# Kernel optimization log

Measured on AMD Instinct MI355X. Metric: run time of the kernel, lower is better.

## Reference

```python
import jax, jax.numpy as jnp
import numpy as np

NEG_SLOPE = 0.2  # PyG GATConv default leaky_relu slope

def gat_conv(x, src, dst, W, att_src, att_dst, bias, concat):
    # x: [N, F_in]; W: [F_in, H*D]; att_*: [H, D]; edges src->dst
    N = x.shape[0]
    H, D = att_src.shape
    h = (x @ W).reshape(N, H, D)                      # [N, H, D]
    a_src = (h * att_src[None]).sum(-1)               # [N, H]
    a_dst = (h * att_dst[None]).sum(-1)               # [N, H]
    e = jax.nn.leaky_relu(a_src[src] + a_dst[dst], NEG_SLOPE)  # [E, H]
    # segment softmax over incoming edges of each destination node
    emax = jax.ops.segment_max(e, dst, num_segments=N)          # [N, H]
    emax = jnp.where(jnp.isfinite(emax), emax, 0.0)
    ex = jnp.exp(e - emax[dst])                                  # [E, H]
    denom = jax.ops.segment_sum(ex, dst, num_segments=N)        # [N, H]
    alpha = ex / (denom[dst] + 1e-16)                            # [E, H]
    msg = h[src] * alpha[:, :, None]                             # [E, H, D]
    out = jax.ops.segment_sum(msg, dst, num_segments=N)          # [N, H, D]
    out = out.reshape(N, H * D) if concat else out.mean(axis=1)
    return out + bias

def setup_inputs() -> dict:
    key = jax.random.key(0)
    ks = jax.random.split(key, 10)
    N, F_in, E, H, D, C = 100000, 128, 3200000, 8, 8, 7
    x = jax.random.normal(ks[0], (N, F_in), jnp.float32)
    edge_index = jax.random.randint(ks[1], (2, E), 0, N, jnp.int64)
    W1 = jax.random.normal(ks[2], (F_in, H * D), jnp.float32) / np.sqrt(F_in)
    att_src1 = jax.random.normal(ks[3], (H, D), jnp.float32) / np.sqrt(D)
    att_dst1 = jax.random.normal(ks[4], (H, D), jnp.float32) / np.sqrt(D)
    b1 = jax.random.normal(ks[5], (H * D,), jnp.float32) * 0.01
    W2 = jax.random.normal(ks[6], (H * D, C), jnp.float32) / np.sqrt(H * D)
    att_src2 = jax.random.normal(ks[7], (1, C), jnp.float32) / np.sqrt(C)
    att_dst2 = jax.random.normal(ks[8], (1, C), jnp.float32) / np.sqrt(C)
    b2 = jax.random.normal(ks[9], (C,), jnp.float32) * 0.01
    return {"x": x, "edge_index": edge_index, "W1": W1, "att_src1": att_src1,
            "att_dst1": att_dst1, "b1": b1, "W2": W2, "att_src2": att_src2,
            "att_dst2": att_dst2, "b2": b2}

def reference(x, edge_index, W1, att_src1, att_dst1, b1, W2, att_src2, att_dst2, b2):
    N = x.shape[0]
    # PyG GATConv add_self_loops=True
    loop = jnp.arange(N, dtype=edge_index.dtype)
    src = jnp.concatenate([edge_index[0], loop])
    dst = jnp.concatenate([edge_index[1], loop])
    # eval mode: dropouts are no-ops
    h = gat_conv(x, src, dst, W1, att_src1, att_dst1, b1, concat=True)
    emb = h
    h = jax.nn.elu(h)
    logits = gat_conv(h, src, dst, W2, att_src2, att_dst2, b2, concat=False)
    return emb, jax.nn.log_softmax(logits, axis=1)
```

## Files before the change

### kernel.cpp

```cpp
#include <hip/hip_runtime.h>
#include <hip/hip_bf16.h>
#include <math.h>

#define F_IN 128
#define HD   64
#define NH   8
#define DH   8
#define NC   7

__device__ __forceinline__ float lrelu(float e) { return fmaxf(e, 0.2f * e); }
__device__ __forceinline__ ushort f2bf(float f) {
    unsigned u = __float_as_uint(f);
    unsigned rounded = u + 0x7FFF + ((u >> 16) & 1);
    return (ushort)(rounded >> 16);
}

__global__ __launch_bounds__(256) void k_gemm1h(
    const float* __restrict__ x, const float* __restrict__ W1,
    const float* __restrict__ att_src, const float* __restrict__ att_dst,
    ushort* __restrict__ h1b, float* __restrict__ a_src, float* __restrict__ a_dst,
    int N, int GB,
    const int* __restrict__ dstArr, int* __restrict__ deg, int* __restrict__ rank,
    long E)
{
    __shared__ float sX[64 * F_IN];
    int t = threadIdx.x;
    int bid = blockIdx.x;

    if (bid % 3 != 0) {
        long hb = (long)(bid / 3) * 2 + (bid % 3) - 1;
        long stride = (long)(2 * GB) * 256;
        for (long i = hb * 256 + t; i < E; i += stride)
            rank[i] = atomicAdd(&deg[dstArr[i]], 1);
        return;
    }

    int gb = bid / 3;
    int lane = t & 63;
    int wave = t >> 6;

    {
        float4 xv[8];
        int r0b = gb * 64;
        #pragma unroll
        for (int i = 0; i < 8; ++i) {
            int ch = i * 256 + t;
            int rr = r0b + (ch >> 5);
            if (rr >= N) rr = N - 1;
            xv[i] = *(const float4*)(x + (size_t)rr * F_IN + ((ch & 31) << 2));
        }
        #pragma unroll
        for (int i = 0; i < 8; ++i) {
            int ch = i * 256 + t;
            *(float4*)(sX + ch * 4) = xv[i];
        }
    }
    float asv = att_src[lane];
    float adv = att_dst[lane];
    __syncthreads();

    int base = gb * 64 + wave * 16;

    #pragma unroll 1
    for (int it = 0; it < 2; ++it) {
        int r0 = base + it * 8;
        if (r0 >= N) break;
        int nr = N - r0; if (nr > 8) nr = 8;
        int lr = wave * 16 + it * 8;

        float acc[8];
        #pragma unroll
        for (int r = 0; r < 8; ++r) acc[r] = 0.f;

        #pragma unroll 1
        for (int kh = 0; kh < 2; ++kh) {
            float wreg[64];
            #pragma unroll
            for (int k = 0; k < 64; ++k)
                wreg[k] = W1[(kh * 64 + k) * HD + lane];

            const float* xb = sX + lr * F_IN + kh * 64;
            #pragma unroll
            for (int k4 = 0; k4 < 16; ++k4) {
                float4 xv[8];
                #pragma unroll
                for (int r = 0; r < 8; ++r)
                    xv[r] = *(const float4*)(xb + r * F_IN + k4 * 4);
                #pragma unroll
                for (int kk = 0; kk < 4; ++kk) {
                    float w = wreg[k4 * 4 + kk];
                    acc[0] += ((const float*)&xv[0])[kk] * w;
                    acc[1] += ((const float*)&xv[1])[kk] * w;
                    acc[2] += ((const float*)&xv[2])[kk] * w;
                    acc[3] += ((const float*)&xv[3])[kk] * w;
                    acc[4] += ((const float*)&xv[4])[kk] * w;
                    acc[5] += ((const float*)&xv[5])[kk] * w;
                    acc[6] += ((const float*)&xv[6])[kk] * w;
                    acc[7] += ((const float*)&xv[7])[kk] * w;
                }
            }
        }

        #pragma unroll
        for (int r = 0; r < 8; ++r) {
            if (r < nr) {
                int row = r0 + r;
                float a = acc[r];
                h1b[(size_t)row * HD + lane] = f2bf(a);
                float vs = a * asv;
                float vd = a * adv;
                #pragma unroll
                for (int o = 4; o > 0; o >>= 1) {
                    vs += __shfl_down(vs, o, 8);
                    vd += __shfl_down(vd, o, 8);
                }
                if ((lane & 7) == 0) {
                    int h = lane >> 3;
                    a_src[row * NH + h] = vs;
                    a_dst[row * NH + h] = vd;
                }
            }
        }
    }
}

__global__ __launch_bounds__(256) void k_bsum(
    const int* __restrict__ deg, int* __restrict__ bsum, int N)
{
    __shared__ int s[256];
    int t = threadIdx.x;
    int i = blockIdx.x * 256 + t;
    s[t] = (i < N) ? deg[i] : 0;
    __syncthreads();
    #pragma unroll
    for (int o = 128; o > 0; o >>= 1) {
        if (t < o) s[t] += s[t + o];
        __syncthreads();
    }
    if (t == 0) bsum[blockIdx.x] = s[0];
}

__global__ __launch_bounds__(512) void k_scan_bsum(
    const int* __restrict__ bsum, int* __restrict__ bexc, int NB)
{
    __shared__ int s[512];
    int t = threadIdx.x;
    s[t] = (t < NB) ? bsum[t] : 0;
    __syncthreads();
    for (int o = 1; o < 512; o <<= 1) {
        int v = (t >= o) ? s[t - o] : 0;
        __syncthreads();
        s[t] += v;
        __syncthreads();
    }
    if (t < NB) bexc[t] = (t == 0) ? 0 : s[t - 1];
}

__global__ __launch_bounds__(256) void k_rowptr(
    const int* __restrict__ deg, const int* __restrict__ bexc,
    int* __restrict__ rowptr, int N, int Etot)
{
    __shared__ int s[256];
    int t = threadIdx.x;
    int i = blockIdx.x * 256 + t;
    int v = (i < N) ? deg[i] : 0;
    s[t] = v;
    __syncthreads();
    for (int o = 1; o < 256; o <<= 1) {
        int u = (t >= o) ? s[t - o] : 0;
        __syncthreads();
        s[t] += u;
        __syncthreads();
    }
    if (i < N) rowptr[i] = bexc[blockIdx.x] + s[t] - v;
    if (i == 0) rowptr[N] = Etot;
}

__global__ __launch_bounds__(256) void k_fill(
    const int* __restrict__ src, const int* __restrict__ dst,
    const int* __restrict__ rank, const int* __restrict__ rowptr,
    int* __restrict__ csr, long E)
{
    long i = (long)blockIdx.x * 256 + threadIdx.x;
    if (i >= E) return;
    csr[rowptr[dst[i]] + rank[i]] = src[i];
}

__global__ __launch_bounds__(256) void k_gather1(
    const int* __restrict__ rowptr, const int* __restrict__ csr,
    const ushort* __restrict__ h1b, const float* __restrict__ a_src,
    const float* __restrict__ a_dst, float* __restrict__ agg, int N)
{
    const uint* __restrict__ h1u = (const uint*)h1b;
    int wave = threadIdx.x >> 6, lane = threadIdx.x & 63;
    int d = blockIdx.x * 4 + wave;
    if (d >= N) return;
    int e = lane >> 3;
    int h = lane & 7;

    float adst = a_dst[d * NH + h];
    float ws = __expf(lrelu(a_src[d * NH + h] + adst));
    float wsum = (e == 0) ? ws : 0.f;

    float ax0 = 0.f, ay0 = 0.f, ax1 = 0.f, ay1 = 0.f;
    float ax2 = 0.f, ay2 = 0.f, ax3 = 0.f, ay3 = 0.f;
    if (e == 0) {
        size_t b = (size_t)d * 32 + h * 4;
        uint u0 = h1u[b], u1 = h1u[b + 1], u2 = h1u[b + 2], u3 = h1u[b + 3];
        ax0 = ws * __uint_as_float(u0 << 16); ay0 = ws * __uint_as_float(u0 & 0xFFFF0000u);
        ax1 = ws * __uint_as_float(u1 << 16); ay1 = ws * __uint_as_float(u1 & 0xFFFF0000u);
        ax2 = ws * __uint_as_float(u2 << 16); ay2 = ws * __uint_as_float(u2 & 0xFFFF0000u);
        ax3 = ws * __uint_as_float(u3 << 16); ay3 = ws * __uint_as_float(u3 & 0xFFFF0000u);
    }

    int jb = rowptr[d], je = rowptr[d + 1];
    int  idx0   = jb + e;
    bool v_cur  = idx0 < je;
    int  sl_cur = v_cur ? csr[idx0] : d;
    float as_cur = a_src[sl_cur * NH + h];

    for (int j0 = jb; j0 < je; j0 += 8) {
        int  idxn  = j0 + 8 + e;
        bool v_n   = idxn < je;
        int  sl_n  = v_n ? csr[idxn] : d;
        float as_n = a_src[sl_n * NH + h];

        float w = v_cur ? __expf(lrelu(as_cur + adst)) : 0.f;
        wsum += w;
        size_t b = (size_t)sl_cur * 32 + h * 4;
        uint u0 = h1u[b], u1 = h1u[b + 1], u2 = h1u[b + 2], u3 = h1u[b + 3];
        ax0 += w * __uint_as_float(u0 << 16); ay0 += w * __uint_as_float(u0 & 0xFFFF0000u);
        ax1 += w * __uint_as_float(u1 << 16); ay1 += w * __uint_as_float(u1 & 0xFFFF0000u);
        ax2 += w * __uint_as_float(u2 << 16); ay2 += w * __uint_as_float(u2 & 0xFFFF0000u);
        ax3 += w * __uint_as_float(u3 << 16); ay3 += w * __uint_as_float(u3 & 0xFFFF0000u);

        sl_cur = sl_n; as_cur = as_n; v_cur = v_n;
    }

    #pragma unroll
    for (int o = 8; o <= 32; o <<= 1) {
        wsum += __shfl_xor(wsum, o, 64);
        ax0 += __shfl_xor(ax0, o, 64); ay0 += __shfl_xor(ay0, o, 64);
        ax1 += __shfl_xor(ax1, o, 64); ay1 += __shfl_xor(ay1, o, 64);
        ax2 += __shfl_xor(ax2, o, 64); ay2 += __shfl_xor(ay2, o, 64);
        ax3 += __shfl_xor(ax3, o, 64); ay3 += __shfl_xor(ay3, o, 64);
    }
    if (e == 0) {
        float winv = 1.f / (wsum + 1e-16f);
        float* op = agg + (size_t)d * HD + h * 8;
        *(float4*)(op)     = make_float4(ax0 * winv, ay0 * winv, ax1 * winv, ay1 * winv);
        *(float4*)(op + 4) = make_float4(ax2 * winv, ay2 * winv, ax3 * winv, ay3 * winv);
    }
}

__global__ __launch_bounds__(256) void k_node2(
    const float* __restrict__ agg1, const float* __restrict__ b1,
    const float* __restrict__ W2, const float* __restrict__ att_s2,
    const float* __restrict__ att_d2, float* __restrict__ emb_out,
    float* __restrict__ h2p, float* __restrict__ a_src2, float* __restrict__ a_dst2,
    int N)
{
    __shared__ float sW[HD * NC];
    __shared__ float sb[HD];
    __shared__ float sas[NC], sad[NC];
    int t = threadIdx.x;
    for (int i = t; i < HD * NC; i += 256) sW[i] = W2[i];
    if (t < HD) sb[t] = b1[t];
    if (t < NC) { sas[t] = att_s2[t]; sad[t] = att_d2[t]; }
    __syncthreads();
    int n = blockIdx.x * 256 + t;
    if (n >= N) return;
    const float* ag = agg1 + (size_t)n * HD;
    float* eo = emb_out + (size_t)n * HD;
    float acc[NC];
    #pragma unroll
    for (int c = 0; c < NC; ++c) acc[c] = 0.f;
    #pragma unroll 8
    for (int k = 0; k < HD; ++k) {
        float v = ag[k] + sb[k];
        eo[k] = v;
        float xv = v > 0.f ? v : expm1f(v);
        #pragma unroll
        for (int c = 0; c < NC; ++c) acc[c] += xv * sW[k * NC + c];
    }
    float as = 0.f, ad = 0.f;
    float* hp = h2p + (size_t)n * 8;
    #pragma unroll
    for (int c = 0; c < NC; ++c) {
        hp[c] = acc[c];
        as += acc[c] * sas[c];
        ad += acc[c] * sad[c];
    }
    hp[7] = 0.f;
    a_src2[n] = as;
    a_dst2[n] = ad;
}

__global__ __launch_bounds__(256) void k_gather2(
    const int* __restrict__ rowptr, const int* __restrict__ csr,
    const float* __restrict__ h2p, const float* __restrict__ a_src2,
    const float* __restrict__ a_dst2, const float* __restrict__ b2,
    float* __restrict__ out, int N)
{
    int t = threadIdx.x;
    int wave = t >> 6, lane = t & 63;
    int g = lane >> 3;
    int c = lane & 7;
    int n = blockIdx.x * 4 + wave;
    if (n >= N) return;
    float ad = a_dst2[n];
    float w = __expf(lrelu(a_src2[n] + ad));
    float acc  = (g == 0) ? w * h2p[(size_t)n * 8 + c] : 0.f;
    float wsum = (g == 0) ? w : 0.f;
    int jb = rowptr[n], je = rowptr[n + 1];

    int  idx0  = jb + g;
    bool v_cur = idx0 < je;
    int  s_cur = v_cur ? csr[idx0] : n;

    for (int j = jb; j < je; j += 8) {
        int  idxn  = j + 8 + g;
        bool v_n   = idxn < je;
        int  s_n   = v_n ? csr[idxn] : n;
        float ww = v_cur ? __expf(lrelu(a_src2[s_cur] + ad)) : 0.f;
        acc += ww * h2p[(size_t)s_cur * 8 + c];
        wsum += ww;
        s_cur = s_n; v_cur = v_n;
    }
    #pragma unroll
    for (int o = 32; o >= 8; o >>= 1) {
        acc  += __shfl_xor(acc, o, 64);
        wsum += __shfl_xor(wsum, o, 64);
    }
    float l = (c < NC) ? (acc / (wsum + 1e-16f) + b2[c]) : -1e30f;
    float m = l;
    #pragma unroll
    for (int o = 4; o > 0; o >>= 1) m = fmaxf(m, __shfl_xor(m, o, 8));
    float ex = (c < NC) ? __expf(l - m) : 0.f;
    float s8 = ex;
    #pragma unroll
    for (int o = 4; o > 0; o >>= 1) s8 += __shfl_xor(s8, o, 8);
    if (g == 0 && c < NC) out[(size_t)n * NC + c] = l - m - logf(s8);
}

extern "C" void kernel_launch(void* const* d_in, const int* in_sizes, int n_in,
                              void* d_out, int out_size, void* d_ws, size_t ws_size,
                              hipStream_t stream)
{
    const float* x       = (const float*)d_in[0];
    const int*   ei      = (const int*)d_in[1];
    const float* W1      = (const float*)d_in[2];
    const float* att_s1  = (const float*)d_in[3];
    const float* att_d1  = (const float*)d_in[4];
    const float* b1      = (const float*)d_in[5];
    const float* W2      = (const float*)d_in[6];
    const float* att_s2  = (const float*)d_in[7];
    const float* att_d2  = (const float*)d_in[8];
    const float* b2      = (const float*)d_in[9];

    const int  N = in_sizes[0] / F_IN;
    const long E = (long)in_sizes[1] / 2;
    const int* src = ei;
    const int* dst = ei + E;

    const int Npad  = (N + 3) & ~3;
    const int Np1p  = (N + 4) & ~3;
    const long Epad = (E + 3) & ~3;

    int* deg    = (int*)d_ws;
    int* rowptr = deg + Npad;
    int* bexc   = rowptr + Np1p;
    int* bsum   = bexc + 512;
    int* csr    = bsum + 512;
    ushort* h1b   = (ushort*)(csr + Epad);
    float* a_src1 = (float*)(h1b + (size_t)Npad * HD);
    float* a_dst1 = a_src1 + (size_t)N * NH;
    float* agg1   = a_dst1 + (size_t)N * NH;
    float* h2p    = agg1 + (size_t)N * HD;
    float* a_src2 = h2p + (size_t)N * 8;
    float* a_dst2 = a_src2 + Npad;
    float* wsend  = a_dst2 + Npad;
    int* rank = (E <= (long)N * HD) ? (int*)agg1 : (int*)wsend;

    hipMemsetAsync(deg, 0, (size_t)Npad * sizeof(int), stream);

    const int NB = (N + 255) / 256;
    const int GB = (N + 63) / 64;
    dim3 b256(256);

    k_gemm1h<<<dim3(3 * GB), b256, 0, stream>>>(
        x, W1, att_s1, att_d1, h1b, a_src1, a_dst1, N, GB,
        dst, deg, rank, E);
    k_bsum<<<dim3(NB), b256, 0, stream>>>(deg, bsum, N);
    k_scan_bsum<<<dim3(1), dim3(512), 0, stream>>>(bsum, bexc, NB);
    k_rowptr<<<dim3(NB), b256, 0, stream>>>(deg, bexc, rowptr, N, (int)E);
    k_fill<<<dim3((unsigned)((E + 255) / 256)), b256, 0, stream>>>(
        src, dst, rank, rowptr, csr, E);

    k_gather1<<<dim3((N + 3) / 4), b256, 0, stream>>>(
        rowptr, csr, h1b, a_src1, a_dst1, agg1, N);

    float* emb = (float*)d_out;
    float* lsm = emb + (size_t)N * HD;
    k_node2<<<dim3(NB), b256, 0, stream>>>(
        agg1, b1, W2, att_s2, att_d2, emb, h2p, a_src2, a_dst2, N);

    k_gather2<<<dim3((N + 3) / 4), b256, 0, stream>>>(
        rowptr, csr, h2p, a_src2, a_dst2, b2, lsm, N);
}
```

Baseline: 641.4 us.

## Use 512-thread blocks for fused GEMM1 and degree counting with int4 edges

The fused GEMM1/degree-count kernel now runs with 512-thread blocks and interleaves GEMM and histogram blocks by odd/even block index instead of a 1:2 ratio. Each histogram thread handles four consecutive edges with one int4 load and one int4 rank store, not a grid-stride loop. Each GEMM wave now computes 8 rows in four 32-wide K chunks, so the W1 register tile is smaller. This aims to cut load instruction count, register pressure and loop overhead, at the cost of a different occupancy profile and some idle blocks when GB and HB differ.

```diff
diff --git a/kernel.cpp b/kernel.cpp
--- a/kernel.cpp
+++ b/kernel.cpp
@@ -15,11 +15,11 @@
     return (ushort)(rounded >> 16);
 }
 
-__global__ __launch_bounds__(256) void k_gemm1h(
+__global__ __launch_bounds__(512, 4) void k_gemm1h(
     const float* __restrict__ x, const float* __restrict__ W1,
     const float* __restrict__ att_src, const float* __restrict__ att_dst,
     ushort* __restrict__ h1b, float* __restrict__ a_src, float* __restrict__ a_dst,
-    int N, int GB,
+    int N, int GB, int HB,
     const int* __restrict__ dstArr, int* __restrict__ deg, int* __restrict__ rank,
     long E)
 {
@@ -27,31 +27,43 @@
     int t = threadIdx.x;
     int bid = blockIdx.x;
 
-    if (bid % 3 != 0) {
-        long hb = (long)(bid / 3) * 2 + (bid % 3) - 1;
-        long stride = (long)(2 * GB) * 256;
-        for (long i = hb * 256 + t; i < E; i += stride)
-            rank[i] = atomicAdd(&deg[dstArr[i]], 1);
+    if (bid & 1) {
+        long hb = bid >> 1;
+        if (hb >= HB) return;
+        long base = hb * 2048 + (long)t * 4;
+        if (base >= E) return;
+        if (base + 3 < E) {
+            int4 d4 = *(const int4*)(dstArr + base);
+            int r0_ = atomicAdd(&deg[d4.x], 1);
+            int r1_ = atomicAdd(&deg[d4.y], 1);
+            int r2_ = atomicAdd(&deg[d4.z], 1);
+            int r3_ = atomicAdd(&deg[d4.w], 1);
+            *(int4*)(rank + base) = make_int4(r0_, r1_, r2_, r3_);
+        } else {
+            for (long i = base; i < E; ++i)
+                rank[i] = atomicAdd(&deg[dstArr[i]], 1);
+        }
         return;
     }
 
-    int gb = bid / 3;
+    int gb = bid >> 1;
+    if (gb >= GB) return;
     int lane = t & 63;
     int wave = t >> 6;
 
     {
-        float4 xv[8];
+        float4 xv[4];
         int r0b = gb * 64;
         #pragma unroll
-        for (int i = 0; i < 8; ++i) {
-            int ch = i * 256 + t;
+        for (int i = 0; i < 4; ++i) {
+            int ch = i * 512 + t;
             int rr = r0b + (ch >> 5);
             if (rr >= N) rr = N - 1;
             xv[i] = *(const float4*)(x + (size_t)rr * F_IN + ((ch & 31) << 2));
         }
         #pragma unroll
-        for (int i = 0; i < 8; ++i) {
-            int ch = i * 256 + t;
+        for (int i = 0; i < 4; ++i) {
+            int ch = i * 512 + t;
             *(float4*)(sX + ch * 4) = xv[i];
         }
     }
@@ -59,33 +71,28 @@
     float adv = att_dst[lane];
     __syncthreads();
 
-    int base = gb * 64 + wave * 16;
-
-    #pragma unroll 1
-    for (int it = 0; it < 2; ++it) {
-        int r0 = base + it * 8;
-        if (r0 >= N) break;
-        int nr = N - r0; if (nr > 8) nr = 8;
-        int lr = wave * 16 + it * 8;
+    int r0 = gb * 64 + wave * 8;
+    if (r0 >= N) goto done;
+    {
+        const float* xb = sX + (wave * 8) * F_IN;
 
         float acc[8];
         #pragma unroll
         for (int r = 0; r < 8; ++r) acc[r] = 0.f;
 
         #pragma unroll 1
-        for (int kh = 0; kh < 2; ++kh) {
-            float wreg[64];
+        for (int kq = 0; kq < 4; ++kq) {
+            float wreg[32];
             #pragma unroll
-            for (int k = 0; k < 64; ++k)
-                wreg[k] = W1[(kh * 64 + k) * HD + lane];
-
-            const float* xb = sX + lr * F_IN + kh * 64;
+            for (int k = 0; k < 32; ++k)
+                wreg[k] = W1[(kq * 32 + k) * HD + lane];
+
             #pragma unroll
-            for (int k4 = 0; k4 < 16; ++k4) {
+            for (int k4 = 0; k4 < 8; ++k4) {
                 float4 xv[8];
                 #pragma unroll
                 for (int r = 0; r < 8; ++r)
-                    xv[r] = *(const float4*)(xb + r * F_IN + k4 * 4);
+                    xv[r] = *(const float4*)(xb + r * F_IN + kq * 32 + k4 * 4);
                 #pragma unroll
                 for (int kk = 0; kk < 4; ++kk) {
                     float w = wreg[k4 * 4 + kk];
@@ -101,6 +108,7 @@
             }
         }
 
+        int nr = N - r0; if (nr > 8) nr = 8;
         #pragma unroll
         for (int r = 0; r < 8; ++r) {
             if (r < nr) {
@@ -122,6 +130,7 @@
             }
         }
     }
+done: ;
 }
 
 __global__ __launch_bounds__(256) void k_bsum(
@@ -386,10 +395,12 @@
 
     const int NB = (N + 255) / 256;
     const int GB = (N + 63) / 64;
+    const int HB = (int)((E + 2047) / 2048);
+    const int M  = (GB > HB) ? GB : HB;
     dim3 b256(256);
 
-    k_gemm1h<<<dim3(3 * GB), b256, 0, stream>>>(
-        x, W1, att_s1, att_d1, h1b, a_src1, a_dst1, N, GB,
+    k_gemm1h<<<dim3(2 * M), dim3(512), 0, stream>>>(
+        x, W1, att_s1, att_d1, h1b, a_src1, a_dst1, N, GB, HB,
         dst, deg, rank, E);
     k_bsum<<<dim3(NB), b256, 0, stream>>>(deg, bsum, N);
     k_scan_bsum<<<dim3(1), dim3(512), 0, stream>>>(bsum, bexc, NB);
```

Result: slower. 703.1 us (+9.6%).
